# Optimization experiments

Measured on AMD Instinct MI355X. Metric: run time of the kernel, lower is better.

## Reference

```python
import jax, jax.numpy as jnp
import numpy as np

ALPHA = 0.2  # LeakyReLU negative slope
NEG_INF = -9e15


def setup_inputs() -> dict:
    key = jax.random.key(0)
    k1, k2, k3, k4 = jax.random.split(key, 4)
    B, N, Fin, Fout = 4, 4096, 128, 64
    x = jax.random.normal(k1, (B, N, Fin), dtype=jnp.float32)
    adj = jax.random.randint(k2, (B, N, N), 0, 2, dtype=jnp.int32)
    # xavier_uniform-ish init scale
    W = jax.random.normal(k3, (Fin, Fout), dtype=jnp.float32) * (1.414 / np.sqrt(Fin + Fout))
    a = jax.random.normal(k4, (3 * Fout, 1), dtype=jnp.float32) * (1.414 / np.sqrt(3 * Fout + 1))
    return {"x": x, "adj": adj, "W": W, "a": a}


def reference(x, adj, W, a):
    # h: [B, N, Fout]
    h = jnp.matmul(x, W)
    Fout = W.shape[1]
    # Original builds a_input[b,i,j] = [h_i, h_j, h_i*h_j] and dots with a.
    # Decompose a into the three blocks; identical math, no O(N^2*3F) tensor.
    a1 = a[:Fout, 0]            # weights on h_i (self)
    a2 = a[Fout:2 * Fout, 0]    # weights on h_j (neighbor)
    a3 = a[2 * Fout:, 0]        # weights on h_i * h_j (corr)
    s_self = jnp.einsum('bnf,f->bn', h, a1)        # [B,N]
    s_nei = jnp.einsum('bnf,f->bn', h, a2)         # [B,N]
    s_corr = jnp.einsum('bif,bjf->bij', h * a3, h)  # [B,N,N]
    e = s_self[:, :, None] + s_nei[:, None, :] + s_corr
    e = jnp.where(e > 0, e, ALPHA * e)  # LeakyReLU
    att = jnp.where(adj > 0, e, NEG_INF)
    att = jax.nn.softmax(att, axis=-1)
    # dropout=0.0 / eval mode -> no dropout
    h_prime = jnp.matmul(att, h)  # [B,N,Fout]
    return jax.nn.elu(h_prime)    # concat=True
```

## Files before the change

### kernel.cpp

```cpp
#include <hip/hip_runtime.h>


typedef __attribute__((ext_vector_type(4))) float f32x4;
typedef __attribute__((ext_vector_type(4))) _Float16 h16x4;
typedef __attribute__((ext_vector_type(8))) _Float16 h16x8;
typedef __attribute__((ext_vector_type(2))) __fp16 fp16x2;

#define L2E 1.4426950408889634f

__global__ __launch_bounds__(256) void gat_phase1(
    const float* __restrict__ x,
    const float* __restrict__ W,
    const float* __restrict__ a,
    _Float16* __restrict__ h16,
    _Float16* __restrict__ hT16,
    _Float16* __restrict__ q16,
    float* __restrict__ sS,
    float* __restrict__ sN)
{
  __shared__ float xs[32 * 132];
  __shared__ float wt[64 * 132];
  const int tid = threadIdx.x;
  const int bx  = blockIdx.x;
  const int b   = bx >> 7;
  const int n0  = (bx & 127) << 5;
  const float* xb = x + ((size_t)b * 4096 + n0) * 128;

#pragma unroll
  for (int p = 0; p < 4; ++p) {
    int idx = tid + p * 256;
    int row = idx >> 5, c4 = idx & 31;
    float4 v = ((const float4*)(xb + row * 128))[c4];
    *(float4*)&xs[row * 132 + c4 * 4] = v;
  }
#pragma unroll
  for (int p = 0; p < 8; ++p) {
    int idx = tid + p * 256;
    int k = idx >> 4, f4 = idx & 15;
    float4 v = ((const float4*)(W + k * 64))[f4];
    wt[(f4 * 4 + 0) * 132 + k] = v.x;
    wt[(f4 * 4 + 1) * 132 + k] = v.y;
    wt[(f4 * 4 + 2) * 132 + k] = v.z;
    wt[(f4 * 4 + 3) * 132 + k] = v.w;
  }
  __syncthreads();

  const int tx = tid & 15;
  const int ty = tid >> 4;
  float acc[2][4];
#pragma unroll
  for (int r = 0; r < 2; ++r)
#pragma unroll
    for (int f = 0; f < 4; ++f) acc[r][f] = 0.f;

#pragma unroll 4
  for (int k = 0; k < 128; k += 4) {
    float4 xv[2], wv[4];
#pragma unroll
    for (int r = 0; r < 2; ++r) xv[r] = *(const float4*)&xs[(2 * ty + r) * 132 + k];
#pragma unroll
    for (int f = 0; f < 4; ++f) wv[f] = *(const float4*)&wt[(4 * tx + f) * 132 + k];
#pragma unroll
    for (int r = 0; r < 2; ++r)
#pragma unroll
      for (int f = 0; f < 4; ++f)
        acc[r][f] += xv[r].x * wv[f].x + xv[r].y * wv[f].y +
                     xv[r].z * wv[f].z + xv[r].w * wv[f].w;
  }

  float a1r[4], a2r[4], a3r[4];
#pragma unroll
  for (int f = 0; f < 4; ++f) {
    a1r[f] = a[4 * tx + f] * L2E;
    a2r[f] = a[64 + 4 * tx + f] * L2E;
    a3r[f] = a[128 + 4 * tx + f] * L2E;
  }
  const size_t bN = (size_t)b * 4096;
#pragma unroll
  for (int r = 0; r < 2; ++r) {
    float p1 = 0.f, p2 = 0.f;
#pragma unroll
    for (int f = 0; f < 4; ++f) { p1 += acc[r][f] * a1r[f]; p2 += acc[r][f] * a2r[f]; }
#pragma unroll
    for (int m = 1; m < 16; m <<= 1) {
      p1 += __shfl_xor(p1, m, 64);
      p2 += __shfl_xor(p2, m, 64);
    }
    if (tx == 0) {
      int n = n0 + 2 * ty + r;
      sS[bN + n] = p1;
      sN[bN + n] = p2;
    }
  }
#pragma unroll
  for (int r = 0; r < 2; ++r) {
    int n = n0 + 2 * ty + r;
    h16x4 hv, qv;
#pragma unroll
    for (int f = 0; f < 4; ++f) {
      hv[f] = (_Float16)acc[r][f];
      qv[f] = (_Float16)(acc[r][f] * a3r[f]);
    }
    *(h16x4*)&h16[(bN + n) * 64 + 4 * tx] = hv;
    *(h16x4*)&q16[(bN + n) * 64 + 4 * tx] = qv;
  }
  __syncthreads();
  _Float16* hTs = (_Float16*)xs;
#pragma unroll
  for (int f = 0; f < 4; ++f)
#pragma unroll
    for (int r = 0; r < 2; ++r)
      hTs[(4 * tx + f) * 40 + 2 * ty + r] = (_Float16)acc[r][f];
  __syncthreads();
  {
    int f = tid >> 2, part = tid & 3;
    uint4 v = *(uint4*)&hTs[f * 40 + 8 * part];
    *(uint4*)&hT16[((size_t)b * 64 + f) * 4096 + n0 + 8 * part] = v;
  }
}

__global__ __launch_bounds__(256, 4) void gat_phase2(
    const _Float16* __restrict__ h16,
    const _Float16* __restrict__ hT16,
    const _Float16* __restrict__ q16,
    const float* __restrict__ sS,
    const float* __restrict__ sN,
    const int* __restrict__ adj,
    float* __restrict__ Opart,
    float* __restrict__ lpart)
{
  __shared__ _Float16 Kbuf[64 * 72];
  __shared__ _Float16 Tbuf[64 * 72];

  const int tid = threadIdx.x;
  const int w = tid >> 6, lane = tid & 63;
  const int qd = lane >> 4, c = lane & 15;
  const int bx = blockIdx.x;
  const int b = bx & 3;
  const int split = (bx >> 2) & 3;
  const int it = bx >> 4;
  const int i0 = it * 64 + w * 16;
  const int jq0 = split * 1024;
  const size_t bN = (size_t)b * 4096;

  const _Float16* qrow = q16 + (bN + i0 + c) * 64;
  h16x8 Qf0 = *(const h16x8*)(qrow + qd * 8);
  h16x8 Qf1 = *(const h16x8*)(qrow + 32 + qd * 8);
  const float ss = sS[bN + i0 + c];

  const int* adjb = adj + (bN + i0 + c) * 4096 + jq0 + 4 * qd;
  const float* snb = sN + bN + jq0 + 4 * qd;

  const int srow = tid >> 3, sc8 = (tid & 7) * 8;
  const _Float16* hsrc = h16 + (bN + jq0 + srow) * 64 + sc8;
  const _Float16* tsrc = hT16 + ((size_t)b * 64 + srow) * 4096 + jq0 + sc8;

  f32x4 O[4];
#pragma unroll
  for (int ft = 0; ft < 4; ++ft) O[ft] = (f32x4){0.f, 0.f, 0.f, 0.f};
  float lsum = 0.f;

  uint4 kr0 = *(const uint4*)hsrc, kr1 = *(const uint4*)(hsrc + 32 * 64);
  uint4 tr0 = *(const uint4*)tsrc, tr1 = *(const uint4*)(tsrc + 32 * 4096);
  uint4 av[4];
#pragma unroll
  for (int ct = 0; ct < 4; ++ct) av[ct] = *(const uint4*)(adjb + 16 * ct);

  for (int t = 0; t < 16; ++t) {
    const int joff = t * 64;
    __syncthreads();
    *(uint4*)&Kbuf[srow * 72 + sc8] = kr0;
    *(uint4*)&Kbuf[(srow + 32) * 72 + sc8] = kr1;
    *(uint4*)&Tbuf[srow * 72 + sc8] = tr0;
    *(uint4*)&Tbuf[(srow + 32) * 72 + sc8] = tr1;
    __syncthreads();

    uint4 avn[4] = {av[0], av[1], av[2], av[3]};
    if (t < 15) {
      const _Float16* hs = hsrc + (joff + 64) * 64;
      const _Float16* ts = tsrc + (joff + 64);
      kr0 = *(const uint4*)hs; kr1 = *(const uint4*)(hs + 32 * 64);
      tr0 = *(const uint4*)ts; tr1 = *(const uint4*)(ts + 32 * 4096);
#pragma unroll
      for (int ct = 0; ct < 4; ++ct)
        avn[ct] = *(const uint4*)(adjb + joff + 64 + 16 * ct);
    }

#pragma unroll
    for (int ct = 0; ct < 4; ++ct) {
      h16x8 Kf0 = *(const h16x8*)&Kbuf[(16 * ct + c) * 72 + qd * 8];
      h16x8 Kf1 = *(const h16x8*)&Kbuf[(16 * ct + c) * 72 + 32 + qd * 8];
      f32x4 Sv = (f32x4){0.f, 0.f, 0.f, 0.f};
      Sv = __builtin_amdgcn_mfma_f32_16x16x32_f16(Kf0, Qf0, Sv, 0, 0, 0);
      Sv = __builtin_amdgcn_mfma_f32_16x16x32_f16(Kf1, Qf1, Sv, 0, 0, 0);

      f32x4 snv = *(const f32x4*)(snb + joff + 16 * ct);
      f32x4 ev = Sv + snv + ss;
      f32x4 tv = __builtin_elementwise_max(ev, ev * 0.2f);
      float p0 = __builtin_amdgcn_exp2f(tv.x);
      float p1 = __builtin_amdgcn_exp2f(tv.y);
      float p2 = __builtin_amdgcn_exp2f(tv.z);
      float p3 = __builtin_amdgcn_exp2f(tv.w);
      p0 = av[ct].x ? p0 : 0.f;
      p1 = av[ct].y ? p1 : 0.f;
      p2 = av[ct].z ? p2 : 0.f;
      p3 = av[ct].w ? p3 : 0.f;
      lsum += (p0 + p1) + (p2 + p3);
      fp16x2 plo = __builtin_amdgcn_cvt_pkrtz(p0, p1);
      fp16x2 phi = __builtin_amdgcn_cvt_pkrtz(p2, p3);
      h16x4 Pf = (h16x4){(_Float16)plo.x, (_Float16)plo.y,
                         (_Float16)phi.x, (_Float16)phi.y};

#pragma unroll
      for (int ft = 0; ft < 4; ++ft) {
        h16x4 Vf = *(const h16x4*)&Tbuf[(16 * ft + c) * 72 + 16 * ct + 4 * qd];
        O[ft] = __builtin_amdgcn_mfma_f32_16x16x16f16(Vf, Pf, O[ft], 0, 0, 0);
      }
    }
#pragma unroll
    for (int ct = 0; ct < 4; ++ct) av[ct] = avn[ct];
  }

  lsum += __shfl_xor(lsum, 16, 64);
  lsum += __shfl_xor(lsum, 32, 64);

  float* orow = Opart + ((size_t)split * 16384 + bN + i0 + c) * 64;
#pragma unroll
  for (int ft = 0; ft < 4; ++ft)
    *(f32x4*)(orow + 16 * ft + 4 * qd) = O[ft];
  if (lane < 16) lpart[split * 16384 + bN + i0 + c] = lsum;
}

__global__ __launch_bounds__(256) void gat_combine(
    const float* __restrict__ Opart, const float* __restrict__ lpart,
    float* __restrict__ out)
{
  const int tid = threadIdx.x;
  const size_t row = (size_t)blockIdx.x * 16 + (tid >> 4);
  const int f4 = (tid & 15) * 4;
  const size_t R = 16384;
  float l = lpart[row] + lpart[R + row] + lpart[2 * R + row] + lpart[3 * R + row];
  f32x4 o = *(const f32x4*)&Opart[row * 64 + f4];
  o += *(const f32x4*)&Opart[(R + row) * 64 + f4];
  o += *(const f32x4*)&Opart[(2 * R + row) * 64 + f4];
  o += *(const f32x4*)&Opart[(3 * R + row) * 64 + f4];
  float inv = 1.0f / l;
  float4 res;
  float v;
  v = o.x * inv; res.x = v > 0.f ? v : __expf(v) - 1.f;
  v = o.y * inv; res.y = v > 0.f ? v : __expf(v) - 1.f;
  v = o.z * inv; res.z = v > 0.f ? v : __expf(v) - 1.f;
  v = o.w * inv; res.w = v > 0.f ? v : __expf(v) - 1.f;
  *(float4*)&out[row * 64 + f4] = res;
}

extern "C" void kernel_launch(void* const* d_in, const int* in_sizes, int n_in,
                              void* d_out, int out_size, void* d_ws, size_t ws_size,
                              hipStream_t stream) {
  const float* x  = (const float*)d_in[0];
  const int* adj  = (const int*)d_in[1];
  const float* W  = (const float*)d_in[2];
  const float* a  = (const float*)d_in[3];
  float* out = (float*)d_out;

  char* ws = (char*)d_ws;
  _Float16* h16  = (_Float16*)(ws);
  _Float16* hT16 = (_Float16*)(ws + (2u << 20));
  _Float16* q16  = (_Float16*)(ws + (4u << 20));
  float* sS = (float*)(ws + (6u << 20));
  float* sN = (float*)(ws + (6u << 20) + (64u << 10));
  float* Opart = (float*)(ws + (6u << 20) + (128u << 10));
  float* lpart = (float*)(ws + (6u << 20) + (128u << 10) + (16u << 20));

  gat_phase1<<<512, 256, 0, stream>>>(x, W, a, h16, hT16, q16, sS, sN);
  gat_phase2<<<1024, 256, 0, stream>>>(h16, hT16, q16, sS, sN, adj, Opart, lpart);
  gat_combine<<<1024, 256, 0, stream>>>(Opart, lpart, out);
}
```

Measured before the change: 409.8 us.

## Drop LDS staging in attention kernel and read K/V fragments directly from global

In phase2 the shared-memory Kbuf/Tbuf staging and both __syncthreads per tile are removed. Each wave now loads its K and V MFMA fragments straight from global memory, relying on the cache, since the four waves in a block read the same data. Phase1 also stops transposing W into LDS and instead uses a row-major copy with float4 broadcast FMAs. The change trades barrier and LDS traffic for redundant global/L2 loads and the loss of the register prefetch for K/V, which may expose more load latency in the main loop.

Result: slower. 514.1 us (+25.4%).

```diff
diff --git a/kernel.cpp b/kernel.cpp
--- a/kernel.cpp
+++ b/kernel.cpp
@@ -19,7 +19,7 @@
     float* __restrict__ sN)
 {
   __shared__ float xs[32 * 132];
-  __shared__ float wt[64 * 132];
+  __shared__ float ws[128 * 64];
   const int tid = threadIdx.x;
   const int bx  = blockIdx.x;
   const int b   = bx >> 7;
@@ -36,37 +36,28 @@
 #pragma unroll
   for (int p = 0; p < 8; ++p) {
     int idx = tid + p * 256;
-    int k = idx >> 4, f4 = idx & 15;
-    float4 v = ((const float4*)(W + k * 64))[f4];
-    wt[(f4 * 4 + 0) * 132 + k] = v.x;
-    wt[(f4 * 4 + 1) * 132 + k] = v.y;
-    wt[(f4 * 4 + 2) * 132 + k] = v.z;
-    wt[(f4 * 4 + 3) * 132 + k] = v.w;
+    ((float4*)ws)[idx] = ((const float4*)W)[idx];
   }
   __syncthreads();
 
   const int tx = tid & 15;
   const int ty = tid >> 4;
-  float acc[2][4];
-#pragma unroll
-  for (int r = 0; r < 2; ++r)
-#pragma unroll
-    for (int f = 0; f < 4; ++f) acc[r][f] = 0.f;
-
-#pragma unroll 4
+  f32x4 acc0 = (f32x4){0.f, 0.f, 0.f, 0.f};
+  f32x4 acc1 = (f32x4){0.f, 0.f, 0.f, 0.f};
+
+#pragma unroll 8
   for (int k = 0; k < 128; k += 4) {
-    float4 xv[2], wv[4];
-#pragma unroll
-    for (int r = 0; r < 2; ++r) xv[r] = *(const float4*)&xs[(2 * ty + r) * 132 + k];
-#pragma unroll
-    for (int f = 0; f < 4; ++f) wv[f] = *(const float4*)&wt[(4 * tx + f) * 132 + k];
-#pragma unroll
-    for (int r = 0; r < 2; ++r)
-#pragma unroll
-      for (int f = 0; f < 4; ++f)
-        acc[r][f] += xv[r].x * wv[f].x + xv[r].y * wv[f].y +
-                     xv[r].z * wv[f].z + xv[r].w * wv[f].w;
-  }
+    f32x4 x0 = *(const f32x4*)&xs[(2 * ty) * 132 + k];
+    f32x4 x1 = *(const f32x4*)&xs[(2 * ty + 1) * 132 + k];
+    f32x4 w0 = *(const f32x4*)&ws[(k + 0) * 64 + 4 * tx];
+    f32x4 w1 = *(const f32x4*)&ws[(k + 1) * 64 + 4 * tx];
+    f32x4 w2 = *(const f32x4*)&ws[(k + 2) * 64 + 4 * tx];
+    f32x4 w3 = *(const f32x4*)&ws[(k + 3) * 64 + 4 * tx];
+    acc0 += x0.x * w0 + x0.y * w1 + x0.z * w2 + x0.w * w3;
+    acc1 += x1.x * w0 + x1.y * w1 + x1.z * w2 + x1.w * w3;
+  }
+  float acc[2][4] = {{acc0.x, acc0.y, acc0.z, acc0.w},
+                     {acc1.x, acc1.y, acc1.z, acc1.w}};
 
   float a1r[4], a2r[4], a3r[4];
 #pragma unroll
@@ -129,9 +120,6 @@
     float* __restrict__ Opart,
     float* __restrict__ lpart)
 {
-  __shared__ _Float16 Kbuf[64 * 72];
-  __shared__ _Float16 Tbuf[64 * 72];
-
   const int tid = threadIdx.x;
   const int w = tid >> 6, lane = tid & 63;
   const int qd = lane >> 4, c = lane & 15;
@@ -148,53 +136,44 @@
   h16x8 Qf1 = *(const h16x8*)(qrow + 32 + qd * 8);
   const float ss = sS[bN + i0 + c];
 
-  const int* adjb = adj + (bN + i0 + c) * 4096 + jq0 + 4 * qd;
+  const _Float16* kbase = h16 + (bN + jq0 + c) * 64 + qd * 8;
+  const _Float16* vbase = hT16 + ((size_t)b * 64 + c) * 4096 + jq0 + 4 * qd;
+  const int* abase = adj + (bN + i0 + c) * 4096 + jq0 + 4 * qd;
   const float* snb = sN + bN + jq0 + 4 * qd;
-
-  const int srow = tid >> 3, sc8 = (tid & 7) * 8;
-  const _Float16* hsrc = h16 + (bN + jq0 + srow) * 64 + sc8;
-  const _Float16* tsrc = hT16 + ((size_t)b * 64 + srow) * 4096 + jq0 + sc8;
 
   f32x4 O[4];
 #pragma unroll
   for (int ft = 0; ft < 4; ++ft) O[ft] = (f32x4){0.f, 0.f, 0.f, 0.f};
   float lsum = 0.f;
 
-  uint4 kr0 = *(const uint4*)hsrc, kr1 = *(const uint4*)(hsrc + 32 * 64);
-  uint4 tr0 = *(const uint4*)tsrc, tr1 = *(const uint4*)(tsrc + 32 * 4096);
   uint4 av[4];
 #pragma unroll
-  for (int ct = 0; ct < 4; ++ct) av[ct] = *(const uint4*)(adjb + 16 * ct);
+  for (int ct = 0; ct < 4; ++ct) av[ct] = *(const uint4*)(abase + 16 * ct);
 
   for (int t = 0; t < 16; ++t) {
-    const int joff = t * 64;
-    __syncthreads();
-    *(uint4*)&Kbuf[srow * 72 + sc8] = kr0;
-    *(uint4*)&Kbuf[(srow + 32) * 72 + sc8] = kr1;
-    *(uint4*)&Tbuf[srow * 72 + sc8] = tr0;
-    *(uint4*)&Tbuf[(srow + 32) * 72 + sc8] = tr1;
-    __syncthreads();
-
+    const int j0 = t * 64;
     uint4 avn[4] = {av[0], av[1], av[2], av[3]};
     if (t < 15) {
-      const _Float16* hs = hsrc + (joff + 64) * 64;
-      const _Float16* ts = tsrc + (joff + 64);
-      kr0 = *(const uint4*)hs; kr1 = *(const uint4*)(hs + 32 * 64);
-      tr0 = *(const uint4*)ts; tr1 = *(const uint4*)(ts + 32 * 4096);
 #pragma unroll
       for (int ct = 0; ct < 4; ++ct)
-        avn[ct] = *(const uint4*)(adjb + joff + 64 + 16 * ct);
+        avn[ct] = *(const uint4*)(abase + j0 + 64 + 16 * ct);
     }
 
 #pragma unroll
     for (int ct = 0; ct < 4; ++ct) {
-      h16x8 Kf0 = *(const h16x8*)&Kbuf[(16 * ct + c) * 72 + qd * 8];
-      h16x8 Kf1 = *(const h16x8*)&Kbuf[(16 * ct + c) * 72 + 32 + qd * 8];
+      const int j = j0 + 16 * ct;
+      h16x8 Kf0 = *(const h16x8*)(kbase + j * 64);
+      h16x8 Kf1 = *(const h16x8*)(kbase + j * 64 + 32);
+      h16x4 Vf0 = *(const h16x4*)(vbase + (size_t)0 * 65536 + j);
+      h16x4 Vf1 = *(const h16x4*)(vbase + (size_t)1 * 65536 + j);
+      h16x4 Vf2 = *(const h16x4*)(vbase + (size_t)2 * 65536 + j);
+      h16x4 Vf3 = *(const h16x4*)(vbase + (size_t)3 * 65536 + j);
+      f32x4 snv = *(const f32x4*)(snb + j);
+
       f32x4 Sv = (f32x4){0.f, 0.f, 0.f, 0.f};
       Sv = __builtin_amdgcn_mfma_f32_16x16x32_f16(Kf0, Qf0, Sv, 0, 0, 0);
       Sv = __builtin_amdgcn_mfma_f32_16x16x32_f16(Kf1, Qf1, Sv, 0, 0, 0);
 
-      f32x4 snv = *(const f32x4*)(snb + joff + 16 * ct);
       f32x4 ev = Sv + snv + ss;
       f32x4 tv = __builtin_elementwise_max(ev, ev * 0.2f);
       float p0 = __builtin_amdgcn_exp2f(tv.x);
@@ -211,11 +190,10 @@
       h16x4 Pf = (h16x4){(_Float16)plo.x, (_Float16)plo.y,
                          (_Float16)phi.x, (_Float16)phi.y};
 
-#pragma unroll
-      for (int ft = 0; ft < 4; ++ft) {
-        h16x4 Vf = *(const h16x4*)&Tbuf[(16 * ft + c) * 72 + 16 * ct + 4 * qd];
-        O[ft] = __builtin_amdgcn_mfma_f32_16x16x16f16(Vf, Pf, O[ft], 0, 0, 0);
-      }
+      O[0] = __builtin_amdgcn_mfma_f32_16x16x16f16(Vf0, Pf, O[0], 0, 0, 0);
+      O[1] = __builtin_amdgcn_mfma_f32_16x16x16f16(Vf1, Pf, O[1], 0, 0, 0);
+      O[2] = __builtin_amdgcn_mfma_f32_16x16x16f16(Vf2, Pf, O[2], 0, 0, 0);
+      O[3] = __builtin_amdgcn_mfma_f32_16x16x16f16(Vf3, Pf, O[3], 0, 0, 0);
     }
 #pragma unroll
     for (int ct = 0; ct < 4; ++ct) av[ct] = avn[ct];
```
